# Performance work log

Measured on AMD Instinct MI355X. Metric: run time of the kernel, lower is better.

## Reference

```python
import jax, jax.numpy as jnp
import numpy as np

N_HEAD = 16
HEAD_DIM = 128
HIDDEN = 2048
ROPE_BASE = 10000.0
RMS_EPS = 1e-5


def _rms_norm(t, w, eps=RMS_EPS):
    # RMSNorm over last dim with learned scale
    var = jnp.mean(jnp.square(t), axis=-1, keepdims=True)
    return t * jax.lax.rsqrt(var + eps) * w


def _rope_cos_sin(T, dim, base=ROPE_BASE, dtype=jnp.float32):
    inv_freq = 1.0 / (base ** (jnp.arange(0, dim, 2, dtype=jnp.float32) / dim))
    pos = jnp.arange(T, dtype=jnp.float32)
    freqs = pos[:, None] * inv_freq[None, :]  # [T, dim/2]
    return jnp.cos(freqs).astype(dtype), jnp.sin(freqs).astype(dtype)


def _apply_rotary(t, cos, sin):
    # t: [B, T, H, D]; rotate-half (GPT-NeoX style)
    d2 = t.shape[-1] // 2
    t1, t2 = t[..., :d2], t[..., d2:]
    c = cos[None, :, None, :]
    s = sin[None, :, None, :]
    return jnp.concatenate([t1 * c - t2 * s, t1 * s + t2 * c], axis=-1)


def setup_inputs() -> dict:
    key = jax.random.key(0)
    ks = jax.random.split(key, 7)
    B, T = 2, 2048
    w_std = 1.0 / np.sqrt(HIDDEN)
    proj_std = 0.5 / np.sqrt(HIDDEN) / np.sqrt(24)  # hidden_init_std_factor / sqrt(H) / sqrt(L)
    return {
        "x": jax.random.normal(ks[0], (B, T, HIDDEN), jnp.float32),
        "Wq": jax.random.normal(ks[1], (HIDDEN, N_HEAD * HEAD_DIM), jnp.float32) * w_std,
        "Wk": jax.random.normal(ks[2], (HIDDEN, N_HEAD * HEAD_DIM), jnp.float32) * w_std,
        "Wv": jax.random.normal(ks[3], (HIDDEN, N_HEAD * HEAD_DIM), jnp.float32) * w_std,
        "Wg": jax.random.normal(ks[4], (HIDDEN, N_HEAD * HEAD_DIM), jnp.float32) * w_std,
        "Wo": jax.random.normal(ks[5], (N_HEAD * HEAD_DIM, HIDDEN), jnp.float32) * proj_std,
        "q_rms_w": jnp.ones((HEAD_DIM,), jnp.float32),
        "k_rms_w": jnp.ones((HEAD_DIM,), jnp.float32),
        "o_norm_w": jnp.ones((HEAD_DIM,), jnp.float32),
    }


def reference(x, Wq, Wk, Wv, Wg, Wo, q_rms_w, k_rms_w, o_norm_w):
    B, T, _ = x.shape
    H, D = N_HEAD, HEAD_DIM

    q = (x @ Wq).reshape(B, T, H, D)
    k = (x @ Wk).reshape(B, T, H, D)
    v = (x @ Wv).reshape(B, T, H, D)

    # RoPE (no past, offset = 0)
    cos, sin = _rope_cos_sin(T, D, dtype=x.dtype)
    q = _apply_rotary(q, cos, sin)
    k = _apply_rotary(k, cos, sin)

    # QK RMSNorm (per-head-dim affine)
    q = _rms_norm(q, q_rms_w)
    k = _rms_norm(k, k_rms_w)

    # causal SDPA
    scale = 1.0 / np.sqrt(D)
    scores = jnp.einsum("bqhd,bkhd->bhqk", q, k) * scale
    causal = jnp.tril(jnp.ones((T, T), dtype=bool))
    scores = jnp.where(causal[None, None, :, :], scores, jnp.finfo(scores.dtype).min)
    probs = jax.nn.softmax(scores, axis=-1)
    y = jnp.einsum("bhqk,bkhd->bqhd", probs, v)  # [B, T, H, D]

    # output norm + silu gate
    y = _rms_norm(y, o_norm_w)
    gate = (x @ Wg).reshape(B, T, H, D)
    y = y * jax.nn.silu(gate)

    y = y.reshape(B, T, H * D)
    return y @ Wo
```

## Files before the change

### kernel.cpp

```cpp
#include <hip/hip_runtime.h>
#include <hip/hip_bf16.h>
#include <stdint.h>

typedef __bf16 bf16x8 __attribute__((ext_vector_type(8)));
typedef float f32x4 __attribute__((ext_vector_type(4)));
typedef __hip_bfloat16 bf16;

__device__ __forceinline__ void gload16(const void* g, void* l) {
    __builtin_amdgcn_global_load_lds(
        (const __attribute__((address_space(1))) uint32_t*)g,
        (__attribute__((address_space(3))) uint32_t*)l,
        16, 0, 0);
}

__global__ void k_cvt_bf16(const float* __restrict__ in, bf16* __restrict__ out, int n4) {
    int i = blockIdx.x * blockDim.x + threadIdx.x;
    if (i >= n4) return;
    float4 v = reinterpret_cast<const float4*>(in)[i];
    union { bf16 h[4]; uint2 u; } pk;
    pk.h[0] = __float2bfloat16(v.x);
    pk.h[1] = __float2bfloat16(v.y);
    pk.h[2] = __float2bfloat16(v.z);
    pk.h[3] = __float2bfloat16(v.w);
    reinterpret_cast<uint2*>(out)[i] = pk.u;
}

__global__ void k_rope_tbl(float* __restrict__ tbl) {
    int i = blockIdx.x * blockDim.x + threadIdx.x;
    int t = i >> 6, j = i & 63;
    float inv = powf(10000.0f, -(float)j * (1.0f / 64.0f));
    float f = (float)t * inv;
    tbl[t * 128 + j] = cosf(f);
    tbl[t * 128 + 64 + j] = sinf(f);
}

__global__ void k_wtrans(const float* __restrict__ w0, const float* __restrict__ w1,
                         const float* __restrict__ w2, const float* __restrict__ w3,
                         const float* __restrict__ w4, bf16* __restrict__ out) {
    __shared__ float tile[32][33];
    const float* srcs[5] = {w0, w1, w2, w3, w4};
    const float* src = srcs[blockIdx.z];
    bf16* dst = out + (size_t)blockIdx.z * 2048 * 2048;
    int k0 = blockIdx.x * 32, n0 = blockIdx.y * 32;
    int tx = threadIdx.x, ty = threadIdx.y;
#pragma unroll
    for (int i = 0; i < 4; i++)
        tile[ty + 8 * i][tx] = src[(size_t)(k0 + ty + 8 * i) * 2048 + n0 + tx];
    __syncthreads();
#pragma unroll
    for (int i = 0; i < 4; i++)
        dst[(size_t)(n0 + ty + 8 * i) * 2048 + k0 + tx] = __float2bfloat16(tile[tx][ty + 8 * i]);
}

__global__ __launch_bounds__(256) void k_gemm(
    const bf16* __restrict__ A, const bf16* __restrict__ Bt, float* __restrict__ C,
    int M, int N, int K) {
    __shared__ __align__(16) bf16 As[128 * 64];
    __shared__ __align__(16) bf16 Bs[128 * 64];
    int lane = threadIdx.x & 63, wave = threadIdx.x >> 6;
    int g = lane >> 4, cc = lane & 15;
    int wr = wave >> 1, wc = wave & 1;
    size_t m0 = (size_t)blockIdx.x * 128, n0 = (size_t)blockIdx.y * 128;
    const bf16* Ab = A + m0 * K;
    const bf16* Bb = Bt + (size_t)blockIdx.z * N * K + n0 * K;
    float* Cb = C + (size_t)blockIdx.z * M * N + m0 * N + n0;

    f32x4 acc[4][4];
#pragma unroll
    for (int i = 0; i < 4; i++)
#pragma unroll
        for (int j = 0; j < 4; j++) acc[i][j] = {0.f, 0.f, 0.f, 0.f};

    int scol = (lane & 7) * 8;
    for (int k0 = 0; k0 < K; k0 += 64) {
#pragma unroll
        for (int i = 0; i < 4; i++) {
            int ch = wave * 4 + i;
            int row = ch * 8 + (lane >> 3);
            gload16(&Ab[(size_t)row * K + k0 + scol], &As[ch * 512]);
            gload16(&Bb[(size_t)row * K + k0 + scol], &Bs[ch * 512]);
        }
        __syncthreads();
#pragma unroll
        for (int kk = 0; kk < 2; kk++) {
            bf16x8 af[4], bfr[4];
#pragma unroll
            for (int m = 0; m < 4; m++)
                af[m] = *reinterpret_cast<const bf16x8*>(&As[(wr * 64 + m * 16 + cc) * 64 + kk * 32 + g * 8]);
#pragma unroll
            for (int n = 0; n < 4; n++)
                bfr[n] = *reinterpret_cast<const bf16x8*>(&Bs[(wc * 64 + n * 16 + cc) * 64 + kk * 32 + g * 8]);
#pragma unroll
            for (int m = 0; m < 4; m++)
#pragma unroll
                for (int n = 0; n < 4; n++)
                    acc[m][n] = __builtin_amdgcn_mfma_f32_16x16x32_bf16(af[m], bfr[n], acc[m][n], 0, 0, 0);
        }
        __syncthreads();
    }
#pragma unroll
    for (int m = 0; m < 4; m++)
#pragma unroll
        for (int n = 0; n < 4; n++)
#pragma unroll
            for (int r = 0; r < 4; r++) {
                size_t row = wr * 64 + m * 16 + g * 4 + r;
                Cb[row * N + (wc * 64 + n * 16 + cc)] = acc[m][n][r];
            }
}

__global__ __launch_bounds__(512, 2) void k_gemm256(
    const bf16* __restrict__ A, const bf16* __restrict__ Bt, bf16* __restrict__ C,
    int M, int N, int K) {
    __shared__ __align__(16) bf16 lds[2][8][64 * 64];
    const int tid = threadIdx.x;
    const int lane = tid & 63, wave = tid >> 6;
    const int g = lane >> 4, c = lane & 15, cx = c & 7;
    const int wr = wave >> 2, wc = wave & 3;
    const int id = blockIdx.x;
    const int swz = (id & 7) * 64 + (id >> 3);
    const int xt = swz & 15, yt = (swz >> 4) & 7, zt = swz >> 7;
    const size_t m0 = (size_t)xt * 256, n0 = (size_t)yt * 256;
    const bf16* Ab = A + m0 * K;
    const bf16* Bb = Bt + (size_t)zt * (size_t)N * K + n0 * K;
    bf16* Cb = C + (size_t)zt * (size_t)M * N + m0 * N + n0;
    const int nt = K >> 6;

    const int srow = tid >> 3;
    const int scol = ((tid & 7) ^ (srow & 7)) * 8;

    auto stage = [&](int u, int q) {
        if (u >= nt) return;
        const bf16* src = (q < 4) ? &Ab[(size_t)(q * 64 + srow) * K]
                                  : &Bb[(size_t)((q - 4) * 64 + srow) * K];
        gload16(&src[((size_t)u << 6) + scol], &lds[u & 1][q][wave * 512]);
    };

    f32x4 acc[8][4];
#pragma unroll
    for (int i = 0; i < 8; i++)
#pragma unroll
        for (int j = 0; j < 4; j++) acc[i][j] = {0.f, 0.f, 0.f, 0.f};

#pragma unroll
    for (int q = 0; q < 8; q++) stage(0, q);
    stage(1, 0); stage(1, 2); stage(1, 4); stage(1, 5); stage(1, 6); stage(1, 7);
    asm volatile("s_waitcnt vmcnt(6)" ::: "memory");
    __builtin_amdgcn_s_barrier();

    bf16x8 afr[4][2], bfr[2][2][2];

#define READ_A(mh)                                                                   \
    do {                                                                             \
        const bf16* aq = &lds[t & 1][wr * 2 + (mh)][0];                              \
        _Pragma("unroll") for (int m_ = 0; m_ < 4; m_++)                             \
            _Pragma("unroll") for (int kh = 0; kh < 2; kh++)                         \
                afr[m_][kh] = *reinterpret_cast<const bf16x8*>(                      \
                    aq + (m_ * 16 + c) * 64 + ((kh * 4 + g) ^ cx) * 8);              \
    } while (0)
#define READ_B(nh)                                                                   \
    do {                                                                             \
        const bf16* bq = &lds[t & 1][4 + wc][0];                                     \
        _Pragma("unroll") for (int n_ = 0; n_ < 2; n_++)                             \
            _Pragma("unroll") for (int kh = 0; kh < 2; kh++)                         \
                bfr[nh][n_][kh] = *reinterpret_cast<const bf16x8*>(                  \
                    bq + (((nh)*2 + n_) * 16 + c) * 64 + ((kh * 4 + g) ^ cx) * 8);   \
    } while (0)
#define QUAD(mh, nh)                                                                 \
    do {                                                                             \
        __builtin_amdgcn_s_setprio(1);                                               \
        _Pragma("unroll") for (int kh = 0; kh < 2; kh++)                             \
            _Pragma("unroll") for (int m_ = 0; m_ < 4; m_++)                         \
                _Pragma("unroll") for (int n_ = 0; n_ < 2; n_++)                     \
                    acc[(mh)*4 + m_][(nh)*2 + n_] =                                  \
                        __builtin_amdgcn_mfma_f32_16x16x32_bf16(                     \
                            afr[m_][kh], bfr[nh][n_][kh],                            \
                            acc[(mh)*4 + m_][(nh)*2 + n_], 0, 0, 0);                 \
        __builtin_amdgcn_s_setprio(0);                                               \
    } while (0)

    for (int t = 0; t < nt; ++t) {
        READ_A(0);
        READ_B(0);
        stage(t + 1, 1); stage(t + 1, 3);
        __builtin_amdgcn_s_barrier();
        asm volatile("s_waitcnt lgkmcnt(0)" ::: "memory");
        __builtin_amdgcn_sched_barrier(0);
        QUAD(0, 0);
        __builtin_amdgcn_s_barrier();
        READ_B(1);
        stage(t + 2, 0); stage(t + 2, 2);
        __builtin_amdgcn_s_barrier();
        asm volatile("s_waitcnt lgkmcnt(0)" ::: "memory");
        __builtin_amdgcn_sched_barrier(0);
        QUAD(0, 1);
        __builtin_amdgcn_s_barrier();
        READ_A(1);
        stage(t + 2, 4); stage(t + 2, 5);
        __builtin_amdgcn_s_barrier();
        asm volatile("s_waitcnt lgkmcnt(0)" ::: "memory");
        __builtin_amdgcn_sched_barrier(0);
        QUAD(1, 0);
        __builtin_amdgcn_s_barrier();
        stage(t + 2, 6); stage(t + 2, 7);
        if (t < nt - 2) asm volatile("s_waitcnt vmcnt(6)" ::: "memory");
        else            asm volatile("s_waitcnt vmcnt(0)" ::: "memory");
        __builtin_amdgcn_s_barrier();
        __builtin_amdgcn_sched_barrier(0);
        QUAD(1, 1);
        __builtin_amdgcn_s_barrier();
    }
#undef READ_A
#undef READ_B
#undef QUAD
#pragma unroll
    for (int m_ = 0; m_ < 8; m_++)
#pragma unroll
        for (int n_ = 0; n_ < 4; n_++)
#pragma unroll
            for (int r_ = 0; r_ < 4; r_++) {
                size_t row = wr * 128 + m_ * 16 + g * 4 + r_;
                Cb[row * N + wc * 64 + n_ * 16 + c] = __float2bfloat16(acc[m_][n_][r_]);
            }
}

__global__ void k_rope_rms(const bf16* __restrict__ src_q, const bf16* __restrict__ src_k,
                           const float* __restrict__ qw, const float* __restrict__ kw,
                           const float* __restrict__ tbl, bf16* __restrict__ dst_q,
                           bf16* __restrict__ dst_k) {
    const int T = 2048;
    int role = blockIdx.y;
    const bf16* src = role ? src_k : src_q;
    const float* rmsw = role ? kw : qw;
    bf16* dst = role ? dst_k : dst_q;
    float outscale = role ? 1.0f : 0.08838834764831845f;
    int wv = blockIdx.x * 4 + (threadIdx.x >> 6);
    int lane = threadIdx.x & 63;
    int h = wv & 15, bt = wv >> 4;
    int t = bt & (T - 1), b_ = bt >> 11;
    const bf16* p = src + (size_t)bt * 2048 + h * 128;
    float a = __bfloat162float(p[lane]), b = __bfloat162float(p[lane + 64]);
    float cs = tbl[t * 128 + lane], sn = tbl[t * 128 + 64 + lane];
    float r1 = a * cs - b * sn, r2 = a * sn + b * cs;
    float ss = r1 * r1 + r2 * r2;
#pragma unroll
    for (int d = 1; d < 64; d <<= 1) ss += __shfl_xor(ss, d, 64);
    float rs = rsqrtf(ss * (1.0f / 128.0f) + 1e-5f);
    size_t o = ((size_t)(b_ * 16 + h) * T + t) * 128;
    dst[o + lane] = __float2bfloat16(r1 * rs * rmsw[lane] * outscale);
    dst[o + lane + 64] = __float2bfloat16(r2 * rs * rmsw[lane + 64] * outscale);
}

__global__ void k_vtrans(const bf16* __restrict__ V, bf16* __restrict__ Vt) {
    const int T = 2048;
    __shared__ float tile[32][33];
    int bh = blockIdx.z, b_ = bh >> 4, h = bh & 15;
    int t0 = blockIdx.x * 32, d0 = blockIdx.y * 32;
    int tx = threadIdx.x, ty = threadIdx.y;
#pragma unroll
    for (int i = 0; i < 4; i++)
        tile[ty + 8 * i][tx] =
            __bfloat162float(V[((size_t)(b_ * T + t0 + ty + 8 * i)) * 2048 + h * 128 + d0 + tx]);
    __syncthreads();
#pragma unroll
    for (int i = 0; i < 4; i++)
        Vt[((size_t)bh * 128 + d0 + ty + 8 * i) * T + t0 + tx] = __float2bfloat16(tile[tx][ty + 8 * i]);
}

__global__ __launch_bounds__(256) void k_attn(
    const bf16* __restrict__ Q, const bf16* __restrict__ K,
    const bf16* __restrict__ Vt, const bf16* __restrict__ gate,
    const float* __restrict__ ow, bf16* __restrict__ out) {
    const int T = 2048;
    __shared__ __align__(16) bf16 KsB[2][64 * 128];
    __shared__ __align__(16) bf16 VsB[2][128 * 64];
    __shared__ __align__(16) bf16 Ps[64 * 72];
    int lane = threadIdx.x & 63, wave = threadIdx.x >> 6;
    int g = lane >> 4, c = lane & 15;
    int wg = blockIdx.x;
    int bh = wg & 31;
    int qt = 31 - (wg >> 5);
    int q0 = qt * 64;
    const bf16* Qb = Q + (size_t)bh * T * 128;
    const bf16* Kb = K + (size_t)bh * T * 128;
    const bf16* Vb = Vt + (size_t)bh * 128 * T;

    int qrow = q0 + wave * 16 + c;
    bf16x8 qf[4];
#pragma unroll
    for (int kk = 0; kk < 4; kk++)
        qf[kk] = *reinterpret_cast<const bf16x8*>(&Qb[(size_t)qrow * 128 + kk * 32 + g * 8]);

    int kli = lane >> 4;
    int vli = lane >> 3;
    int vlu = (lane & 7) ^ (vli & 7);

    auto stage = [&](int kv0, int b) {
#pragma unroll
        for (int i = 0; i < 4; i++) {
            int ch = wave * 4 + i;
            int krow = ch * 4 + kli;
            int klu = (lane & 15) ^ (krow & 7);
            gload16(&Kb[(size_t)(kv0 + krow) * 128 + klu * 8], &KsB[b][ch * 512]);
            int vrow = ch * 8 + vli;
            gload16(&Vb[(size_t)vrow * T + kv0 + vlu * 8], &VsB[b][ch * 512]);
        }
    };

    f32x4 acc[8];
#pragma unroll
    for (int i = 0; i < 8; i++) acc[i] = {0.f, 0.f, 0.f, 0.f};
    float m = -INFINITY, l = 0.f;

    int ntiles = qt + 1;
    stage(0, 0);
    __syncthreads();
    int cur = 0;
    for (int it = 0; it < ntiles; ++it) {
        int kv0 = it * 64;
        if (it + 1 < ntiles) stage(kv0 + 64, cur ^ 1);
        const bf16* Ks = KsB[cur];
        const bf16* Vs = VsB[cur];

        f32x4 s[4];
#pragma unroll
        for (int nf = 0; nf < 4; nf++) s[nf] = {0.f, 0.f, 0.f, 0.f};
#pragma unroll
        for (int nf = 0; nf < 4; nf++)
#pragma unroll
            for (int kk = 0; kk < 4; kk++) {
                int pu = (kk * 4 + g) ^ (c & 7);
                bf16x8 kf = *reinterpret_cast<const bf16x8*>(&Ks[(nf * 16 + c) * 128 + pu * 8]);
                s[nf] = __builtin_amdgcn_mfma_f32_16x16x32_bf16(kf, qf[kk], s[nf], 0, 0, 0);
            }
        if (it == ntiles - 1) {
#pragma unroll
            for (int nf = 0; nf < 4; nf++)
#pragma unroll
                for (int r = 0; r < 4; r++)
                    if (kv0 + nf * 16 + g * 4 + r > qrow) s[nf][r] = -1e30f;
        }
        float mx = -INFINITY;
#pragma unroll
        for (int nf = 0; nf < 4; nf++)
#pragma unroll
            for (int r = 0; r < 4; r++) mx = fmaxf(mx, s[nf][r]);
        mx = fmaxf(mx, __shfl_xor(mx, 16, 64));
        mx = fmaxf(mx, __shfl_xor(mx, 32, 64));
        if (__all(mx - m <= 8.0f)) {
            float rsum = 0.f;
#pragma unroll
            for (int nf = 0; nf < 4; nf++)
#pragma unroll
                for (int r = 0; r < 4; r++) {
                    float p = __expf(s[nf][r] - m);
                    s[nf][r] = p;
                    rsum += p;
                }
            rsum += __shfl_xor(rsum, 16, 64);
            rsum += __shfl_xor(rsum, 32, 64);
            l += rsum;
        } else {
            float mnew = fmaxf(m, mx);
            float alpha = __expf(m - mnew);
            m = mnew;
            float rsum = 0.f;
#pragma unroll
            for (int nf = 0; nf < 4; nf++)
#pragma unroll
                for (int r = 0; r < 4; r++) {
                    float p = __expf(s[nf][r] - mnew);
                    s[nf][r] = p;
                    rsum += p;
                }
            rsum += __shfl_xor(rsum, 16, 64);
            rsum += __shfl_xor(rsum, 32, 64);
            l = l * alpha + rsum;
            float al[4];
#pragma unroll
            for (int r = 0; r < 4; r++) al[r] = __shfl(alpha, g * 4 + r, 64);
#pragma unroll
            for (int nf = 0; nf < 8; nf++)
#pragma unroll
                for (int r = 0; r < 4; r++) acc[nf][r] *= al[r];
        }
#pragma unroll
        for (int nf = 0; nf < 4; nf++) {
            union { bf16 h[4]; uint2 u; } pk;
#pragma unroll
            for (int r = 0; r < 4; r++) pk.h[r] = __float2bfloat16(s[nf][r]);
            *reinterpret_cast<uint2*>(&Ps[(wave * 16 + c) * 72 + nf * 16 + g * 4]) = pk.u;
        }
#pragma unroll
        for (int kk2 = 0; kk2 < 2; kk2++) {
            bf16x8 pf = *reinterpret_cast<const bf16x8*>(&Ps[(wave * 16 + c) * 72 + kk2 * 32 + g * 8]);
#pragma unroll
            for (int nf = 0; nf < 8; nf++) {
                int pu = (kk2 * 4 + g) ^ (c & 7);
                bf16x8 vf = *reinterpret_cast<const bf16x8*>(&Vs[(nf * 16 + c) * 64 + pu * 8]);
                acc[nf] = __builtin_amdgcn_mfma_f32_16x16x32_bf16(pf, vf, acc[nf], 0, 0, 0);
            }
        }
        __syncthreads();
        cur ^= 1;
    }
    float inv = 1.0f / l;
    float iv[4];
#pragma unroll
    for (int r = 0; r < 4; r++) iv[r] = __shfl(inv, g * 4 + r, 64);
    int b_ = bh >> 4, h = bh & 15;
    float owv[8];
#pragma unroll
    for (int nf = 0; nf < 8; nf++) owv[nf] = ow[nf * 16 + c];
#pragma unroll
    for (int r = 0; r < 4; r++) {
        int row = q0 + wave * 16 + g * 4 + r;
        float y[8];
        float ss = 0.f;
#pragma unroll
        for (int nf = 0; nf < 8; nf++) {
            y[nf] = acc[nf][r] * iv[r];
            ss += y[nf] * y[nf];
        }
        ss += __shfl_xor(ss, 1, 64);
        ss += __shfl_xor(ss, 2, 64);
        ss += __shfl_xor(ss, 4, 64);
        ss += __shfl_xor(ss, 8, 64);
        float rs = rsqrtf(ss * (1.0f / 128.0f) + 1e-5f);
        size_t gi = ((size_t)(b_ * T + row)) * 2048 + h * 128;
#pragma unroll
        for (int nf = 0; nf < 8; nf++) {
            int col = nf * 16 + c;
            float gv = __bfloat162float(gate[gi + col]);
            gv = gv / (1.f + __expf(-gv));
            out[gi + col] = __float2bfloat16(y[nf] * rs * owv[nf] * gv);
        }
    }
}

extern "C" void kernel_launch(void* const* d_in, const int* in_sizes, int n_in,
                              void* d_out, int out_size, void* d_ws, size_t ws_size,
                              hipStream_t stream) {
    const float* x  = (const float*)d_in[0];
    const float* Wq = (const float*)d_in[1];
    const float* Wk = (const float*)d_in[2];
    const float* Wv = (const float*)d_in[3];
    const float* Wg = (const float*)d_in[4];
    const float* Wo = (const float*)d_in[5];
    const float* qw = (const float*)d_in[6];
    const float* kw = (const float*)d_in[7];
    const float* ow = (const float*)d_in[8];

    const size_t M = 4096, HID = 2048;
    char* w = (char*)d_ws;
    bf16*  xb    = (bf16*)(w);
    bf16*  Wt    = (bf16*)(w + 16777216);
    bf16*  qkvg  = (bf16*)(w + 58720256);
    bf16*  q_att = (bf16*)(w + 125829120);
    bf16*  k_att = (bf16*)(w + 142606336);
    bf16*  vt    = (bf16*)(w + 159383552);
    float* tbl   = (float*)(w + 176160768);
    bf16*  yg    = (bf16*)(w + 177209344);

    k_cvt_bf16<<<8192, 256, 0, stream>>>(x, xb, (int)(M * HID / 4));
    k_rope_tbl<<<512, 256, 0, stream>>>(tbl);
    k_wtrans<<<dim3(64, 64, 5), dim3(32, 8), 0, stream>>>(Wq, Wk, Wv, Wg, Wo, Wt);
    k_gemm256<<<512, 512, 0, stream>>>(xb, Wt, qkvg, (int)M, 2048, 2048);
    k_rope_rms<<<dim3(16384, 2), 256, 0, stream>>>(qkvg, qkvg + M * HID, qw, kw, tbl,
                                                   q_att, k_att);
    k_vtrans<<<dim3(64, 4, 32), dim3(32, 8), 0, stream>>>(qkvg + 2 * M * HID, vt);
    k_attn<<<1024, 256, 0, stream>>>(q_att, k_att, vt, qkvg + 3 * M * HID, ow, yg);
    k_gemm<<<dim3(32, 16, 1), 256, 0, stream>>>(yg, Wt + (size_t)4 * 2048 * 2048, (float*)d_out,
                                                (int)M, 2048, 2048);
}
```

Before: 314.8 us.

## Use 128-row query tiles with 8 waves, keep P in registers

The attention kernel now runs 512 threads per block and covers 128 query rows per block. This halves the number of times each K/V tile is loaded per query, and waves skip key tiles that lie entirely above their causal diagonal. K rows in shared memory are permuted so the QK^T accumulator layout feeds the PV MFMA directly from registers, which removes the Ps shared-memory round trip. The weight transpose also switches to 64x64 tiles. The risks are fewer blocks to balance across CUs and idle waves on diagonal tiles.

```diff
diff --git a/kernel.cpp b/kernel.cpp
--- a/kernel.cpp
+++ b/kernel.cpp
@@ -37,19 +37,19 @@
 __global__ void k_wtrans(const float* __restrict__ w0, const float* __restrict__ w1,
                          const float* __restrict__ w2, const float* __restrict__ w3,
                          const float* __restrict__ w4, bf16* __restrict__ out) {
-    __shared__ float tile[32][33];
+    __shared__ float tile[64][65];
     const float* srcs[5] = {w0, w1, w2, w3, w4};
     const float* src = srcs[blockIdx.z];
     bf16* dst = out + (size_t)blockIdx.z * 2048 * 2048;
-    int k0 = blockIdx.x * 32, n0 = blockIdx.y * 32;
+    int k0 = blockIdx.x * 64, n0 = blockIdx.y * 64;
     int tx = threadIdx.x, ty = threadIdx.y;
 #pragma unroll
-    for (int i = 0; i < 4; i++)
-        tile[ty + 8 * i][tx] = src[(size_t)(k0 + ty + 8 * i) * 2048 + n0 + tx];
+    for (int i = 0; i < 16; i++)
+        tile[ty + 4 * i][tx] = src[(size_t)(k0 + ty + 4 * i) * 2048 + n0 + tx];
     __syncthreads();
 #pragma unroll
-    for (int i = 0; i < 4; i++)
-        dst[(size_t)(n0 + ty + 8 * i) * 2048 + k0 + tx] = __float2bfloat16(tile[tx][ty + 8 * i]);
+    for (int i = 0; i < 16; i++)
+        dst[(size_t)(n0 + ty + 4 * i) * 2048 + k0 + tx] = __float2bfloat16(tile[tx][ty + 4 * i]);
 }
 
 __global__ __launch_bounds__(256) void k_gemm(
@@ -267,20 +267,19 @@
         Vt[((size_t)bh * 128 + d0 + ty + 8 * i) * T + t0 + tx] = __float2bfloat16(tile[tx][ty + 8 * i]);
 }
 
-__global__ __launch_bounds__(256) void k_attn(
+__global__ __launch_bounds__(512) void k_attn(
     const bf16* __restrict__ Q, const bf16* __restrict__ K,
     const bf16* __restrict__ Vt, const bf16* __restrict__ gate,
     const float* __restrict__ ow, bf16* __restrict__ out) {
     const int T = 2048;
     __shared__ __align__(16) bf16 KsB[2][64 * 128];
     __shared__ __align__(16) bf16 VsB[2][128 * 64];
-    __shared__ __align__(16) bf16 Ps[64 * 72];
     int lane = threadIdx.x & 63, wave = threadIdx.x >> 6;
     int g = lane >> 4, c = lane & 15;
     int wg = blockIdx.x;
     int bh = wg & 31;
-    int qt = 31 - (wg >> 5);
-    int q0 = qt * 64;
+    int qt = 15 - (wg >> 5);
+    int q0 = qt * 128;
     const bf16* Qb = Q + (size_t)bh * T * 128;
     const bf16* Kb = K + (size_t)bh * T * 128;
     const bf16* Vb = Vt + (size_t)bh * 128 * T;
@@ -291,19 +290,22 @@
     for (int kk = 0; kk < 4; kk++)
         qf[kk] = *reinterpret_cast<const bf16x8*>(&Qb[(size_t)qrow * 128 + kk * 32 + g * 8]);
 
-    int kli = lane >> 4;
-    int vli = lane >> 3;
-    int vlu = (lane & 7) ^ (vli & 7);
-
+    int kprow[2], klu[2], vrow[2], vlu[2];
+#pragma unroll
+    for (int i = 0; i < 2; i++) {
+        int ch = wave * 2 + i;
+        int p = ch * 4 + (lane >> 4);
+        kprow[i] = ((p >> 5) & 1) * 32 + ((p >> 2) & 3) * 8 + ((p >> 4) & 1) * 4 + (p & 3);
+        klu[i] = (lane & 15) ^ (p & 7);
+        vrow[i] = ch * 8 + (lane >> 3);
+        vlu[i] = (lane & 7) ^ (vrow[i] & 7);
+    }
     auto stage = [&](int kv0, int b) {
 #pragma unroll
-        for (int i = 0; i < 4; i++) {
-            int ch = wave * 4 + i;
-            int krow = ch * 4 + kli;
-            int klu = (lane & 15) ^ (krow & 7);
-            gload16(&Kb[(size_t)(kv0 + krow) * 128 + klu * 8], &KsB[b][ch * 512]);
-            int vrow = ch * 8 + vli;
-            gload16(&Vb[(size_t)vrow * T + kv0 + vlu * 8], &VsB[b][ch * 512]);
+        for (int i = 0; i < 2; i++) {
+            int ch = wave * 2 + i;
+            gload16(&Kb[(size_t)(kv0 + kprow[i]) * 128 + klu[i] * 8], &KsB[b][ch * 512]);
+            gload16(&Vb[(size_t)vrow[i] * T + kv0 + vlu[i] * 8], &VsB[b][ch * 512]);
         }
     };
 
@@ -312,93 +314,94 @@
     for (int i = 0; i < 8; i++) acc[i] = {0.f, 0.f, 0.f, 0.f};
     float m = -INFINITY, l = 0.f;
 
-    int ntiles = qt + 1;
+    int ntiles = 2 * qt + 2;
     stage(0, 0);
     __syncthreads();
     int cur = 0;
     for (int it = 0; it < ntiles; ++it) {
         int kv0 = it * 64;
         if (it + 1 < ntiles) stage(kv0 + 64, cur ^ 1);
-        const bf16* Ks = KsB[cur];
-        const bf16* Vs = VsB[cur];
-
-        f32x4 s[4];
-#pragma unroll
-        for (int nf = 0; nf < 4; nf++) s[nf] = {0.f, 0.f, 0.f, 0.f};
-#pragma unroll
-        for (int nf = 0; nf < 4; nf++)
-#pragma unroll
-            for (int kk = 0; kk < 4; kk++) {
-                int pu = (kk * 4 + g) ^ (c & 7);
-                bf16x8 kf = *reinterpret_cast<const bf16x8*>(&Ks[(nf * 16 + c) * 128 + pu * 8]);
-                s[nf] = __builtin_amdgcn_mfma_f32_16x16x32_bf16(kf, qf[kk], s[nf], 0, 0, 0);
+        if (kv0 <= q0 + wave * 16 + 15) {
+            const bf16* Ks = KsB[cur];
+            const bf16* Vs = VsB[cur];
+
+            f32x4 s[4];
+#pragma unroll
+            for (int nf = 0; nf < 4; nf++) s[nf] = {0.f, 0.f, 0.f, 0.f};
+#pragma unroll
+            for (int nf = 0; nf < 4; nf++)
+#pragma unroll
+                for (int kk = 0; kk < 4; kk++) {
+                    int pu = (kk * 4 + g) ^ (c & 7);
+                    bf16x8 kf = *reinterpret_cast<const bf16x8*>(&Ks[(nf * 16 + c) * 128 + pu * 8]);
+                    s[nf] = __builtin_amdgcn_mfma_f32_16x16x32_bf16(kf, qf[kk], s[nf], 0, 0, 0);
+                }
+            if (kv0 + 63 > q0 + wave * 16) {
+#pragma unroll
+                for (int nf = 0; nf < 4; nf++)
+#pragma unroll
+                    for (int r = 0; r < 4; r++)
+                        if (kv0 + (nf >> 1) * 32 + g * 8 + (nf & 1) * 4 + r > qrow)
+                            s[nf][r] = -1e30f;
             }
-        if (it == ntiles - 1) {
+            float mx = -INFINITY;
 #pragma unroll
             for (int nf = 0; nf < 4; nf++)
 #pragma unroll
-                for (int r = 0; r < 4; r++)
-                    if (kv0 + nf * 16 + g * 4 + r > qrow) s[nf][r] = -1e30f;
-        }
-        float mx = -INFINITY;
-#pragma unroll
-        for (int nf = 0; nf < 4; nf++)
-#pragma unroll
-            for (int r = 0; r < 4; r++) mx = fmaxf(mx, s[nf][r]);
-        mx = fmaxf(mx, __shfl_xor(mx, 16, 64));
-        mx = fmaxf(mx, __shfl_xor(mx, 32, 64));
-        if (__all(mx - m <= 8.0f)) {
-            float rsum = 0.f;
-#pragma unroll
-            for (int nf = 0; nf < 4; nf++)
+                for (int r = 0; r < 4; r++) mx = fmaxf(mx, s[nf][r]);
+            mx = fmaxf(mx, __shfl_xor(mx, 16, 64));
+            mx = fmaxf(mx, __shfl_xor(mx, 32, 64));
+            if (__all(mx - m <= 8.0f)) {
+                float rsum = 0.f;
+#pragma unroll
+                for (int nf = 0; nf < 4; nf++)
+#pragma unroll
+                    for (int r = 0; r < 4; r++) {
+                        float p = __expf(s[nf][r] - m);
+                        s[nf][r] = p;
+                        rsum += p;
+                    }
+                rsum += __shfl_xor(rsum, 16, 64);
+                rsum += __shfl_xor(rsum, 32, 64);
+                l += rsum;
+            } else {
+                float mnew = fmaxf(m, mx);
+                float alpha = __expf(m - mnew);
+                m = mnew;
+                float rsum = 0.f;
+#pragma unroll
+                for (int nf = 0; nf < 4; nf++)
+#pragma unroll
+                    for (int r = 0; r < 4; r++) {
+                        float p = __expf(s[nf][r] - mnew);
+                        s[nf][r] = p;
+                        rsum += p;
+                    }
+                rsum += __shfl_xor(rsum, 16, 64);
+                rsum += __shfl_xor(rsum, 32, 64);
+                l = l * alpha + rsum;
+                float al[4];
+#pragma unroll
+                for (int r = 0; r < 4; r++) al[r] = __shfl(alpha, g * 4 + r, 64);
+#pragma unroll
+                for (int nf = 0; nf < 8; nf++)
+#pragma unroll
+                    for (int r = 0; r < 4; r++) acc[nf][r] *= al[r];
+            }
+#pragma unroll
+            for (int kk2 = 0; kk2 < 2; kk2++) {
+                union { bf16 h[8]; bf16x8 v; } pf;
 #pragma unroll
                 for (int r = 0; r < 4; r++) {
-                    float p = __expf(s[nf][r] - m);
-                    s[nf][r] = p;
-                    rsum += p;
+                    pf.h[r] = __float2bfloat16(s[2 * kk2][r]);
+                    pf.h[4 + r] = __float2bfloat16(s[2 * kk2 + 1][r]);
                 }
-            rsum += __shfl_xor(rsum, 16, 64);
-            rsum += __shfl_xor(rsum, 32, 64);
-            l += rsum;
-        } else {
-            float mnew = fmaxf(m, mx);
-            float alpha = __expf(m - mnew);
-            m = mnew;
-            float rsum = 0.f;
-#pragma unroll
-            for (int nf = 0; nf < 4; nf++)
-#pragma unroll
-                for (int r = 0; r < 4; r++) {
-                    float p = __expf(s[nf][r] - mnew);
-                    s[nf][r] = p;
-                    rsum += p;
+#pragma unroll
+                for (int nf = 0; nf < 8; nf++) {
+                    int pu = (kk2 * 4 + g) ^ (c & 7);
+                    bf16x8 vf = *reinterpret_cast<const bf16x8*>(&Vs[(nf * 16 + c) * 64 + pu * 8]);
+                    acc[nf] = __builtin_amdgcn_mfma_f32_16x16x32_bf16(pf.v, vf, acc[nf], 0, 0, 0);
                 }
-            rsum += __shfl_xor(rsum, 16, 64);
-            rsum += __shfl_xor(rsum, 32, 64);
-            l = l * alpha + rsum;
-            float al[4];
-#pragma unroll
-            for (int r = 0; r < 4; r++) al[r] = __shfl(alpha, g * 4 + r, 64);
-#pragma unroll
-            for (int nf = 0; nf < 8; nf++)
-#pragma unroll
-                for (int r = 0; r < 4; r++) acc[nf][r] *= al[r];
-        }
-#pragma unroll
-        for (int nf = 0; nf < 4; nf++) {
-            union { bf16 h[4]; uint2 u; } pk;
-#pragma unroll
-            for (int r = 0; r < 4; r++) pk.h[r] = __float2bfloat16(s[nf][r]);
-            *reinterpret_cast<uint2*>(&Ps[(wave * 16 + c) * 72 + nf * 16 + g * 4]) = pk.u;
-        }
-#pragma unroll
-        for (int kk2 = 0; kk2 < 2; kk2++) {
-            bf16x8 pf = *reinterpret_cast<const bf16x8*>(&Ps[(wave * 16 + c) * 72 + kk2 * 32 + g * 8]);
-#pragma unroll
-            for (int nf = 0; nf < 8; nf++) {
-                int pu = (kk2 * 4 + g) ^ (c & 7);
-                bf16x8 vf = *reinterpret_cast<const bf16x8*>(&Vs[(nf * 16 + c) * 64 + pu * 8]);
-                acc[nf] = __builtin_amdgcn_mfma_f32_16x16x32_bf16(pf, vf, acc[nf], 0, 0, 0);
             }
         }
         __syncthreads();
@@ -464,12 +467,12 @@
 
     k_cvt_bf16<<<8192, 256, 0, stream>>>(x, xb, (int)(M * HID / 4));
     k_rope_tbl<<<512, 256, 0, stream>>>(tbl);
-    k_wtrans<<<dim3(64, 64, 5), dim3(32, 8), 0, stream>>>(Wq, Wk, Wv, Wg, Wo, Wt);
+    k_wtrans<<<dim3(32, 32, 5), dim3(64, 4), 0, stream>>>(Wq, Wk, Wv, Wg, Wo, Wt);
     k_gemm256<<<512, 512, 0, stream>>>(xb, Wt, qkvg, (int)M, 2048, 2048);
     k_rope_rms<<<dim3(16384, 2), 256, 0, stream>>>(qkvg, qkvg + M * HID, qw, kw, tbl,
                                                    q_att, k_att);
     k_vtrans<<<dim3(64, 4, 32), dim3(32, 8), 0, stream>>>(qkvg + 2 * M * HID, vt);
-    k_attn<<<1024, 256, 0, stream>>>(q_att, k_att, vt, qkvg + 3 * M * HID, ow, yg);
+    k_attn<<<512, 512, 0, stream>>>(q_att, k_att, vt, qkvg + 3 * M * HID, ow, yg);
     k_gemm<<<dim3(32, 16, 1), 256, 0, stream>>>(yg, Wt + (size_t)4 * 2048 * 2048, (float*)d_out,
                                                 (int)M, 2048, 2048);
 }
```

Measured after the change: 320.4 us. Within noise of the previous version (+1.8%).
